# Optimization experiments

Hardware: AMD Instinct MI355X
Metric: run time of the kernel (lower is better)

Reference implementation:

```python
import jax, jax.numpy as jnp
from jax import lax
import numpy as np

B, P, M1, M2, M3 = 128, 168, 2, 2, 2
M = M1 * M2 * M3
HIDC, HIDR, HIDS, CK, SKIP, HW = 50, 50, 5, 6, 24, 24
PT = (P - CK) // SKIP  # int((P-Ck)/skip) = 6
L = P - CK + 1         # 163


def gru(xs, w_ih, w_hh, b_ih, b_hh, hid):
    # xs: [T, N, in]; torch nn.GRU cell semantics, h0 = 0. Returns final h: [N, hid].
    def step(h, x):
        gi = x @ w_ih.T + b_ih
        gh = h @ w_hh.T + b_hh
        ir, iz, inn = jnp.split(gi, 3, axis=-1)
        hr, hz, hn = jnp.split(gh, 3, axis=-1)
        r = jax.nn.sigmoid(ir + hr)
        z = jax.nn.sigmoid(iz + hz)
        n = jnp.tanh(inn + r * hn)
        return (1.0 - z) * n + z * h, None
    h0 = jnp.zeros((xs.shape[1], hid), xs.dtype)
    h, _ = lax.scan(step, h0, xs)
    return h


def setup_inputs() -> dict:
    key = jax.random.key(0)
    ks = jax.random.split(key, 16)
    O = P * HIDC * CK  # 50400 conv output channels
    d = {
        'x': jax.random.normal(ks[0], (B, P, M1, M2, M3), jnp.float32),
        'conv_w': jax.random.normal(ks[1], (O, P, M1, M2, M3), jnp.float32) * 0.02,
        'conv_b': jax.random.normal(ks[2], (O,), jnp.float32) * 0.02,
        'g1_wih': jax.random.normal(ks[3], (3 * HIDR, HIDC), jnp.float32) * 0.1,
        'g1_whh': jax.random.normal(ks[4], (3 * HIDR, HIDR), jnp.float32) * 0.1,
        'g1_bih': jax.random.normal(ks[5], (3 * HIDR,), jnp.float32) * 0.1,
        'g1_bhh': jax.random.normal(ks[6], (3 * HIDR,), jnp.float32) * 0.1,
        'gs_wih': jax.random.normal(ks[7], (3 * HIDS, HIDC), jnp.float32) * 0.1,
        'gs_whh': jax.random.normal(ks[8], (3 * HIDS, HIDS), jnp.float32) * 0.1,
        'gs_bih': jax.random.normal(ks[9], (3 * HIDS,), jnp.float32) * 0.1,
        'gs_bhh': jax.random.normal(ks[10], (3 * HIDS,), jnp.float32) * 0.1,
        'l1_w': jax.random.normal(ks[11], (M, HIDR + SKIP * HIDS), jnp.float32) * 0.1,
        'l1_b': jax.random.normal(ks[12], (M,), jnp.float32) * 0.1,
        'hw_w': jax.random.normal(ks[13], (1, HW), jnp.float32) * 0.1,
        'hw_b': jax.random.normal(ks[14], (1,), jnp.float32) * 0.1,
    }
    return d


def reference(x, conv_w, conv_b, g1_wih, g1_whh, g1_bih, g1_bhh,
              gs_wih, gs_whh, gs_bih, gs_bhh, l1_w, l1_b, hw_w, hw_b):
    # Conv3d with kernel == full spatial extent is a dense matmul over (P*m1*m2*m3).
    xf = x.reshape(B, -1)                       # [B, P*M]
    wf = conv_w.reshape(conv_w.shape[0], -1)    # [O, P*M]
    c = jax.nn.relu(xf @ wf.T + conv_b)         # [B, O]
    c = c.reshape(B, HIDC, CK, P)
    # Diagonal strided sum (the torch triple loop): res1[b,c,t] = sum_k c[b,c,k,k+t]
    res1 = sum(c[:, :, k, k:k + L] for k in range(CK))  # [B, HIDC, L]
    # dropout: eval mode (identity)
    r = gru(jnp.transpose(res1, (2, 0, 1)), g1_wih, g1_whh, g1_bih, g1_bhh, HIDR)  # [B, HIDR]
    # skip GRU
    s = res1[:, :, -PT * SKIP:]                          # [B, HIDC, PT*SKIP]
    s = s.reshape(B, HIDC, PT, SKIP)
    s = jnp.transpose(s, (2, 0, 3, 1)).reshape(PT, B * SKIP, HIDC)
    hs = gru(s, gs_wih, gs_whh, gs_bih, gs_bhh, HIDS)    # [B*SKIP, HIDS]
    hs = hs.reshape(B, SKIP * HIDS)
    r = jnp.concatenate([r, hs], axis=1)                 # [B, HIDR + SKIP*HIDS]
    res = r @ l1_w.T + l1_b                              # [B, M]
    # highway (AR) component over the last HW timesteps
    z = x[:, -HW:].reshape(B, HW, M)                     # [B, HW, M]
    z = jnp.transpose(z, (0, 2, 1)).reshape(-1, HW)      # [B*M, HW]
    z = z @ hw_w.T + hw_b                                # [B*M, 1]
    res = res + z.reshape(B, M)
    res = jax.nn.sigmoid(res)
    return res.reshape(B, M1, M2, M3)
```

## Files before the change

### kernel.cpp

```cpp
#include <hip/hip_runtime.h>
#include <hip/hip_bf16.h>
#include <cstdint>


typedef __attribute__((ext_vector_type(8))) short short8;
typedef __attribute__((ext_vector_type(4))) float f32x4;

__device__ __forceinline__ unsigned short bf16rn(float f) {
    unsigned u = __float_as_uint(f);
    return (unsigned short)((u + 0x7FFFu + ((u >> 16) & 1u)) >> 16);
}
__device__ __forceinline__ unsigned pk2(float a, float b) {
    return ((unsigned)bf16rn(b) << 16) | (unsigned)bf16rn(a);
}
__device__ __forceinline__ uint4 pack8(float4 f0, float4 f1) {
    uint4 u;
    u.x = pk2(f0.x, f0.y); u.y = pk2(f0.z, f0.w);
    u.z = pk2(f1.x, f1.y); u.w = pk2(f1.z, f1.w);
    return u;
}
__device__ __forceinline__ float bf2f(unsigned short u) {
    return __uint_as_float((unsigned)u << 16);
}
__device__ __forceinline__ float sigmf(float x) { return 1.f / (1.f + __expf(-x)); }
__device__ __forceinline__ float tanhf_(float x) { return 1.f - 2.f / (__expf(2.f * x) + 1.f); }

__global__ __launch_bounds__(256, 2)
void k1_conv_gemm(const float* __restrict__ x, const float* __restrict__ w,
                  const float* __restrict__ bias, unsigned short* __restrict__ c) {
    __shared__ uint4 a_lds[8 * 129];
    __shared__ uint4 b_lds[8 * 113];
    const int tid  = threadIdx.x;
    const int n0   = blockIdx.x * 112;
    const int wave = tid >> 6, lane = tid & 63;
    const int quad = lane >> 4, m16 = lane & 15;

    f32x4 acc[2][7];
#pragma unroll
    for (int i = 0; i < 2; ++i)
#pragma unroll
        for (int j = 0; j < 7; ++j) acc[i][j] = (f32x4){0.f, 0.f, 0.f, 0.f};

    for (int kb = 0; kb < 1344; kb += 64) {
#pragma unroll
        for (int i = 0; i < 4; ++i) {
            int idx = tid + i * 256;
            int row = idx >> 3, ks = idx & 7;
            const float* gp = x + row * 1344 + kb + ks * 8;
            float4 f0 = *reinterpret_cast<const float4*>(gp);
            float4 f1 = *reinterpret_cast<const float4*>(gp + 4);
            a_lds[ks * 129 + row] = pack8(f0, f1);
        }
#pragma unroll
        for (int i = 0; i < 4; ++i) {
            int idx = tid + i * 256;
            if (idx < 896) {
                int row = idx >> 3, ks = idx & 7;
                const float* gp = w + (size_t)(n0 + row) * 1344 + kb + ks * 8;
                float4 f0 = *reinterpret_cast<const float4*>(gp);
                float4 f1 = *reinterpret_cast<const float4*>(gp + 4);
                b_lds[ks * 113 + row] = pack8(f0, f1);
            }
        }
        __syncthreads();
#pragma unroll
        for (int half = 0; half < 2; ++half) {
            const int kp = half * 4 + quad;
            short8 af[2], bfr[7];
#pragma unroll
            for (int rt = 0; rt < 2; ++rt)
                af[rt] = ((const short8*)a_lds)[kp * 129 + wave * 32 + rt * 16 + m16];
#pragma unroll
            for (int ct = 0; ct < 7; ++ct)
                bfr[ct] = ((const short8*)b_lds)[kp * 113 + ct * 16 + m16];
#pragma unroll
            for (int rt = 0; rt < 2; ++rt)
#pragma unroll
                for (int ct = 0; ct < 7; ++ct)
                    acc[rt][ct] = __builtin_amdgcn_mfma_f32_16x16x32_bf16(
                        af[rt], bfr[ct], acc[rt][ct], 0, 0, 0);
        }
        __syncthreads();
    }
#pragma unroll
    for (int ct = 0; ct < 7; ++ct) {
        int col = n0 + ct * 16 + m16;
        float bv = bias[col];
#pragma unroll
        for (int rt = 0; rt < 2; ++rt) {
#pragma unroll
            for (int r = 0; r < 4; ++r) {
                int grow = wave * 32 + rt * 16 + quad * 4 + r;
                float v = acc[rt][ct][r] + bv;
                v = fmaxf(v, 0.f);
                c[(size_t)grow * 50400 + col] = bf16rn(v);
            }
        }
    }
}

__global__ __launch_bounds__(256)
void k2_diag(const unsigned short* __restrict__ c, float* __restrict__ res1) {
    __shared__ float rloc[50 * 164];
    const int b = blockIdx.x;
    const unsigned short* cb = c + (size_t)b * 50400;
    for (int idx = threadIdx.x; idx < 8150; idx += 256) {
        int hc = idx / 163, t = idx - hc * 163;
        int base = hc * 1008 + t;
        float s = 0.f;
#pragma unroll
        for (int k = 0; k < 6; ++k) s += bf2f(cb[base + 169 * k]);
        rloc[hc * 164 + t] = s;
    }
    __syncthreads();
    for (int idx = threadIdx.x; idx < 8150; idx += 256) {
        int t = idx / 50, hc = idx - t * 50;
        res1[(size_t)(t * 128 + b) * 50 + hc] = rloc[hc * 164 + t];
    }
}

__global__ __launch_bounds__(256)
void k3_gi1(const float* __restrict__ res1, const float* __restrict__ wih,
            const float* __restrict__ bih, float* __restrict__ gi1) {
    __shared__ float wl[150 * 51];
    __shared__ float xl[32 * 50];
    const int row0 = blockIdx.x * 32;
    for (int idx = threadIdx.x; idx < 7500; idx += 256) {
        int r = idx / 50, j = idx - r * 50;
        wl[r * 51 + j] = wih[idx];
    }
    for (int idx = threadIdx.x; idx < 1600; idx += 256)
        xl[idx] = res1[(size_t)row0 * 50 + idx];
    __syncthreads();
    for (int e = threadIdx.x; e < 4800; e += 256) {
        int rr = e / 150, cc = e - rr * 150;
        float acc = bih[cc];
        const float* xp = &xl[rr * 50];
        const float* wp = &wl[cc * 51];
#pragma unroll
        for (int j = 0; j < 50; ++j) acc += xp[j] * wp[j];
        gi1[(size_t)(row0 + rr) * 150 + cc] = acc;
    }
}

__global__ __launch_bounds__(256)
void k3_gi2(const float* __restrict__ res1, const float* __restrict__ wih,
            const float* __restrict__ bih, float* __restrict__ gi2) {
    __shared__ float wl[15 * 51];
    __shared__ float xl[32 * 50];
    const int row0 = blockIdx.x * 32;
    for (int idx = threadIdx.x; idx < 750; idx += 256) {
        int r = idx / 50, j = idx - r * 50;
        wl[r * 51 + j] = wih[idx];
    }
    for (int idx = threadIdx.x; idx < 1600; idx += 256) {
        int rr = idx / 50, j = idx - rr * 50;
        int r = row0 + rr;
        int pt = r / 3072, bsk = r - pt * 3072;
        int b = bsk / 24, sk = bsk - b * 24;
        int t = 19 + pt * 24 + sk;
        xl[idx] = res1[(size_t)(t * 128 + b) * 50 + j];
    }
    __syncthreads();
    for (int e = threadIdx.x; e < 480; e += 256) {
        int rr = e / 15, cc = e - rr * 15;
        float acc = bih[cc];
#pragma unroll
        for (int j = 0; j < 50; ++j) acc += xl[rr * 50 + j] * wl[cc * 51 + j];
        gi2[(size_t)(row0 + rr) * 15 + cc] = acc;
    }
}

__global__ __launch_bounds__(64)
void k4_gru1(const float* __restrict__ gi1, const float* __restrict__ whh,
             const float* __restrict__ bhh, float* __restrict__ r1) {
    __shared__ float wl[7500];
    __shared__ __align__(16) float hl[52];
    const int b = blockIdx.x;
    const int l = threadIdx.x;
    for (int idx = l; idx < 7500; idx += 64) wl[idx] = whh[idx];
    if (l < 52) hl[l] = 0.f;
    __syncthreads();
    const int lc = (l < 50) ? l : 49;
    float wr[50], wz[50], wn[50];
#pragma unroll
    for (int j = 0; j < 50; ++j) {
        wr[j] = wl[lc * 50 + j];
        wz[j] = wl[(50 + lc) * 50 + j];
        wn[j] = wl[(100 + lc) * 50 + j];
    }
    const float bhr = bhh[lc], bhz = bhh[50 + lc], bhn = bhh[100 + lc];
    float hcur = 0.f;
    for (int t = 0; t < 163; ++t) {
        const float* gp = gi1 + ((size_t)t * 128 + b) * 150;
        float gir = gp[lc], giz = gp[50 + lc], gin = gp[100 + lc];
        float ar = bhr, az = bhz, an = bhn;
#pragma unroll
        for (int j4 = 0; j4 < 12; ++j4) {
            float4 hv = *reinterpret_cast<const float4*>(&hl[4 * j4]);
            ar += wr[4 * j4 + 0] * hv.x + wr[4 * j4 + 1] * hv.y +
                  wr[4 * j4 + 2] * hv.z + wr[4 * j4 + 3] * hv.w;
            az += wz[4 * j4 + 0] * hv.x + wz[4 * j4 + 1] * hv.y +
                  wz[4 * j4 + 2] * hv.z + wz[4 * j4 + 3] * hv.w;
            an += wn[4 * j4 + 0] * hv.x + wn[4 * j4 + 1] * hv.y +
                  wn[4 * j4 + 2] * hv.z + wn[4 * j4 + 3] * hv.w;
        }
        {
            float h48 = hl[48], h49 = hl[49];
            ar += wr[48] * h48 + wr[49] * h49;
            az += wz[48] * h48 + wz[49] * h49;
            an += wn[48] * h48 + wn[49] * h49;
        }
        float rg = sigmf(gir + ar);
        float zg = sigmf(giz + az);
        float ng = tanhf_(gin + rg * an);
        float hn = (1.f - zg) * ng + zg * hcur;
        __syncthreads();
        if (l < 50) { hl[l] = hn; hcur = hn; }
        __syncthreads();
    }
    if (l < 50) r1[b * 50 + l] = hcur;
}

__global__ __launch_bounds__(256)
void k5_gru2(const float* __restrict__ gi2, const float* __restrict__ whh,
             const float* __restrict__ bhh, float* __restrict__ hs) {
    __shared__ float wl[75];
    __shared__ float bl[15];
    const int tid = threadIdx.x;
    if (tid < 75) wl[tid] = whh[tid];
    if (tid < 15) bl[tid] = bhh[tid];
    __syncthreads();
    const int bsk = blockIdx.x * 256 + tid;
    float h[5] = {0.f, 0.f, 0.f, 0.f, 0.f};
    for (int pt = 0; pt < 6; ++pt) {
        const float* gp = gi2 + (size_t)(pt * 3072 + bsk) * 15;
        float gi[15];
#pragma unroll
        for (int i = 0; i < 15; ++i) gi[i] = gp[i];
        float gh[15];
#pragma unroll
        for (int i = 0; i < 15; ++i) {
            float s = bl[i];
#pragma unroll
            for (int j = 0; j < 5; ++j) s += wl[i * 5 + j] * h[j];
            gh[i] = s;
        }
#pragma unroll
        for (int u = 0; u < 5; ++u) {
            float rg = sigmf(gi[u] + gh[u]);
            float zg = sigmf(gi[5 + u] + gh[5 + u]);
            float ng = tanhf_(gi[10 + u] + rg * gh[10 + u]);
            h[u] = (1.f - zg) * ng + zg * h[u];
        }
    }
#pragma unroll
    for (int u = 0; u < 5; ++u) hs[bsk * 5 + u] = h[u];
}

__global__ __launch_bounds__(256)
void k6_final(const float* __restrict__ r1, const float* __restrict__ hs,
              const float* __restrict__ l1w, const float* __restrict__ l1b,
              const float* __restrict__ x, const float* __restrict__ hww,
              const float* __restrict__ hwb, float* __restrict__ out) {
    const int tid = blockIdx.x * 256 + threadIdx.x;
    if (tid >= 1024) return;
    const int b = tid >> 3, m = tid & 7;
    float acc = l1b[m];
    const float* wrow = l1w + m * 170;
    const float* rb = r1 + b * 50;
#pragma unroll
    for (int j = 0; j < 50; ++j) acc += rb[j] * wrow[j];
    const float* hb = hs + b * 120;
#pragma unroll
    for (int j = 0; j < 120; ++j) acc += hb[j] * wrow[50 + j];
    float z = hwb[0];
    const float* xb = x + b * 1344 + 144 * 8 + m;
#pragma unroll
    for (int wi = 0; wi < 24; ++wi) z += xb[wi * 8] * hww[wi];
    out[tid] = 1.f / (1.f + __expf(-(acc + z)));
}

extern "C" void kernel_launch(void* const* d_in, const int* in_sizes, int n_in,
                              void* d_out, int out_size, void* d_ws, size_t ws_size,
                              hipStream_t stream) {
    const float* x      = (const float*)d_in[0];
    const float* conv_w = (const float*)d_in[1];
    const float* conv_b = (const float*)d_in[2];
    const float* g1_wih = (const float*)d_in[3];
    const float* g1_whh = (const float*)d_in[4];
    const float* g1_bih = (const float*)d_in[5];
    const float* g1_bhh = (const float*)d_in[6];
    const float* gs_wih = (const float*)d_in[7];
    const float* gs_whh = (const float*)d_in[8];
    const float* gs_bih = (const float*)d_in[9];
    const float* gs_bhh = (const float*)d_in[10];
    const float* l1_w   = (const float*)d_in[11];
    const float* l1_b   = (const float*)d_in[12];
    const float* hw_w   = (const float*)d_in[13];
    const float* hw_b   = (const float*)d_in[14];
    float* out = (float*)d_out;

    char* ws = (char*)d_ws;
    unsigned short* c   = (unsigned short*)(ws);
    float* res1         = (float*)(ws + 12902400);
    float* gi1          = (float*)(ws + 17075200);
    float* gi2          = (float*)(ws + 29593600);
    float* r1           = (float*)(ws + 30699520);
    float* hs           = (float*)(ws + 30725120);

    hipLaunchKernelGGL(k1_conv_gemm, dim3(450), dim3(256), 0, stream, x, conv_w, conv_b, c);
    hipLaunchKernelGGL(k2_diag,      dim3(128), dim3(256), 0, stream, c, res1);
    hipLaunchKernelGGL(k3_gi1,       dim3(652), dim3(256), 0, stream, res1, g1_wih, g1_bih, gi1);
    hipLaunchKernelGGL(k3_gi2,       dim3(576), dim3(256), 0, stream, res1, gs_wih, gs_bih, gi2);
    hipLaunchKernelGGL(k4_gru1,      dim3(128), dim3(64),  0, stream, gi1, g1_whh, g1_bhh, r1);
    hipLaunchKernelGGL(k5_gru2,      dim3(12),  dim3(256), 0, stream, gi2, gs_whh, gs_bhh, hs);
    hipLaunchKernelGGL(k6_final,     dim3(4),   dim3(256), 0, stream, r1, hs, l1_w, l1_b, x, hw_w, hw_b, out);
}
```

Before: 618.0 us.

## Prefetch GEMM tiles into registers, vectorize input projections, double-buffer GRU hidden state

The conv GEMM now loads the next K-tile from global memory into registers while MFMAs run on the current tile, hiding load latency behind compute at the cost of more registers. The input-projection kernels process 64 rows per block with float4-vectorized dot products over padded LDS rows. The GRU1 recurrence double-buffers the hidden state to drop one barrier per step and prefetches the next step's gate inputs. Register pressure in the GEMM could reduce occupancy, and the changed summation order slightly alters floating-point results.

After: 588.1 us. 4.8% less time.

```diff
diff --git a/kernel.cpp b/kernel.cpp
--- a/kernel.cpp
+++ b/kernel.cpp
@@ -41,28 +41,47 @@
 #pragma unroll
         for (int j = 0; j < 7; ++j) acc[i][j] = (f32x4){0.f, 0.f, 0.f, 0.f};
 
+    float4 pa[4][2];
+    float4 pb[4][2];
+
+    auto issue = [&](int kb) {
+#pragma unroll
+        for (int i = 0; i < 4; ++i) {
+            int row = (tid >> 3) + 32 * i;
+            const float* gp = x + row * 1344 + kb + (tid & 7) * 8;
+            pa[i][0] = *reinterpret_cast<const float4*>(gp);
+            pa[i][1] = *reinterpret_cast<const float4*>(gp + 4);
+        }
+#pragma unroll
+        for (int i = 0; i < 4; ++i) {
+            int idx = tid + 256 * i;
+            if (idx < 896) {
+                int row = idx >> 3;
+                const float* gp = w + (size_t)(n0 + row) * 1344 + kb + (idx & 7) * 8;
+                pb[i][0] = *reinterpret_cast<const float4*>(gp);
+                pb[i][1] = *reinterpret_cast<const float4*>(gp + 4);
+            }
+        }
+    };
+
+    issue(0);
     for (int kb = 0; kb < 1344; kb += 64) {
 #pragma unroll
         for (int i = 0; i < 4; ++i) {
-            int idx = tid + i * 256;
+            int idx = tid + 256 * i;
             int row = idx >> 3, ks = idx & 7;
-            const float* gp = x + row * 1344 + kb + ks * 8;
-            float4 f0 = *reinterpret_cast<const float4*>(gp);
-            float4 f1 = *reinterpret_cast<const float4*>(gp + 4);
-            a_lds[ks * 129 + row] = pack8(f0, f1);
+            a_lds[ks * 129 + row] = pack8(pa[i][0], pa[i][1]);
         }
 #pragma unroll
         for (int i = 0; i < 4; ++i) {
-            int idx = tid + i * 256;
+            int idx = tid + 256 * i;
             if (idx < 896) {
                 int row = idx >> 3, ks = idx & 7;
-                const float* gp = w + (size_t)(n0 + row) * 1344 + kb + ks * 8;
-                float4 f0 = *reinterpret_cast<const float4*>(gp);
-                float4 f1 = *reinterpret_cast<const float4*>(gp + 4);
-                b_lds[ks * 113 + row] = pack8(f0, f1);
+                b_lds[ks * 113 + row] = pack8(pb[i][0], pb[i][1]);
             }
         }
         __syncthreads();
+        if (kb + 64 < 1344) issue(kb + 64);
 #pragma unroll
         for (int half = 0; half < 2; ++half) {
             const int kp = half * 4 + quad;
@@ -122,23 +141,32 @@
 __global__ __launch_bounds__(256)
 void k3_gi1(const float* __restrict__ res1, const float* __restrict__ wih,
             const float* __restrict__ bih, float* __restrict__ gi1) {
-    __shared__ float wl[150 * 51];
-    __shared__ float xl[32 * 50];
-    const int row0 = blockIdx.x * 32;
+    __shared__ float wl[150 * 52];
+    __shared__ float xl[64 * 52];
+    const int row0 = blockIdx.x * 64;
     for (int idx = threadIdx.x; idx < 7500; idx += 256) {
         int r = idx / 50, j = idx - r * 50;
-        wl[r * 51 + j] = wih[idx];
-    }
-    for (int idx = threadIdx.x; idx < 1600; idx += 256)
-        xl[idx] = res1[(size_t)row0 * 50 + idx];
-    __syncthreads();
-    for (int e = threadIdx.x; e < 4800; e += 256) {
+        wl[r * 52 + j] = wih[idx];
+    }
+    for (int idx = threadIdx.x; idx < 3200; idx += 256) {
+        int r = idx / 50, j = idx - r * 50;
+        xl[r * 52 + j] = res1[(size_t)row0 * 50 + idx];
+    }
+    __syncthreads();
+    for (int e = threadIdx.x; e < 9600; e += 256) {
         int rr = e / 150, cc = e - rr * 150;
-        float acc = bih[cc];
-        const float* xp = &xl[rr * 50];
-        const float* wp = &wl[cc * 51];
-#pragma unroll
-        for (int j = 0; j < 50; ++j) acc += xp[j] * wp[j];
+        float4 a0 = {0.f, 0.f, 0.f, 0.f};
+        const float* xp = &xl[rr * 52];
+        const float* wp = &wl[cc * 52];
+#pragma unroll
+        for (int j = 0; j < 48; j += 4) {
+            float4 xv = *reinterpret_cast<const float4*>(xp + j);
+            float4 wv = *reinterpret_cast<const float4*>(wp + j);
+            a0.x += xv.x * wv.x; a0.y += xv.y * wv.y;
+            a0.z += xv.z * wv.z; a0.w += xv.w * wv.w;
+        }
+        float acc = bih[cc] + xp[48] * wp[48] + xp[49] * wp[49]
+                  + (a0.x + a0.y) + (a0.z + a0.w);
         gi1[(size_t)(row0 + rr) * 150 + cc] = acc;
     }
 }
@@ -146,27 +174,36 @@
 __global__ __launch_bounds__(256)
 void k3_gi2(const float* __restrict__ res1, const float* __restrict__ wih,
             const float* __restrict__ bih, float* __restrict__ gi2) {
-    __shared__ float wl[15 * 51];
-    __shared__ float xl[32 * 50];
-    const int row0 = blockIdx.x * 32;
+    __shared__ float wl[15 * 52];
+    __shared__ float xl[64 * 52];
+    const int row0 = blockIdx.x * 64;
     for (int idx = threadIdx.x; idx < 750; idx += 256) {
         int r = idx / 50, j = idx - r * 50;
-        wl[r * 51 + j] = wih[idx];
-    }
-    for (int idx = threadIdx.x; idx < 1600; idx += 256) {
+        wl[r * 52 + j] = wih[idx];
+    }
+    for (int idx = threadIdx.x; idx < 3200; idx += 256) {
         int rr = idx / 50, j = idx - rr * 50;
         int r = row0 + rr;
         int pt = r / 3072, bsk = r - pt * 3072;
         int b = bsk / 24, sk = bsk - b * 24;
         int t = 19 + pt * 24 + sk;
-        xl[idx] = res1[(size_t)(t * 128 + b) * 50 + j];
-    }
-    __syncthreads();
-    for (int e = threadIdx.x; e < 480; e += 256) {
+        xl[rr * 52 + j] = res1[(size_t)(t * 128 + b) * 50 + j];
+    }
+    __syncthreads();
+    for (int e = threadIdx.x; e < 960; e += 256) {
         int rr = e / 15, cc = e - rr * 15;
-        float acc = bih[cc];
-#pragma unroll
-        for (int j = 0; j < 50; ++j) acc += xl[rr * 50 + j] * wl[cc * 51 + j];
+        float4 a0 = {0.f, 0.f, 0.f, 0.f};
+        const float* xp = &xl[rr * 52];
+        const float* wp = &wl[cc * 52];
+#pragma unroll
+        for (int j = 0; j < 48; j += 4) {
+            float4 xv = *reinterpret_cast<const float4*>(xp + j);
+            float4 wv = *reinterpret_cast<const float4*>(wp + j);
+            a0.x += xv.x * wv.x; a0.y += xv.y * wv.y;
+            a0.z += xv.z * wv.z; a0.w += xv.w * wv.w;
+        }
+        float acc = bih[cc] + xp[48] * wp[48] + xp[49] * wp[49]
+                  + (a0.x + a0.y) + (a0.z + a0.w);
         gi2[(size_t)(row0 + rr) * 15 + cc] = acc;
     }
 }
@@ -175,11 +212,12 @@
 void k4_gru1(const float* __restrict__ gi1, const float* __restrict__ whh,
              const float* __restrict__ bhh, float* __restrict__ r1) {
     __shared__ float wl[7500];
-    __shared__ __align__(16) float hl[52];
+    __shared__ __align__(16) float hl[2][64];
     const int b = blockIdx.x;
     const int l = threadIdx.x;
     for (int idx = l; idx < 7500; idx += 64) wl[idx] = whh[idx];
-    if (l < 52) hl[l] = 0.f;
+    hl[0][l] = 0.f;
+    hl[1][l] = 0.f;
     __syncthreads();
     const int lc = (l < 50) ? l : 49;
     float wr[50], wz[50], wn[50];
@@ -191,13 +229,20 @@
     }
     const float bhr = bhh[lc], bhz = bhh[50 + lc], bhn = bhh[100 + lc];
     float hcur = 0.f;
+    const float* gp = gi1 + (size_t)b * 150;
+    float gir = gp[lc], giz = gp[50 + lc], gin = gp[100 + lc];
+    int p = 0;
     for (int t = 0; t < 163; ++t) {
-        const float* gp = gi1 + ((size_t)t * 128 + b) * 150;
-        float gir = gp[lc], giz = gp[50 + lc], gin = gp[100 + lc];
+        float ngir = 0.f, ngiz = 0.f, ngin = 0.f;
+        if (t < 162) {
+            const float* gq = gp + 150 * 128;
+            ngir = gq[lc]; ngiz = gq[50 + lc]; ngin = gq[100 + lc];
+        }
+        const float* hp = hl[p];
         float ar = bhr, az = bhz, an = bhn;
 #pragma unroll
         for (int j4 = 0; j4 < 12; ++j4) {
-            float4 hv = *reinterpret_cast<const float4*>(&hl[4 * j4]);
+            float4 hv = *reinterpret_cast<const float4*>(hp + 4 * j4);
             ar += wr[4 * j4 + 0] * hv.x + wr[4 * j4 + 1] * hv.y +
                   wr[4 * j4 + 2] * hv.z + wr[4 * j4 + 3] * hv.w;
             az += wz[4 * j4 + 0] * hv.x + wz[4 * j4 + 1] * hv.y +
@@ -206,7 +251,7 @@
                   wn[4 * j4 + 2] * hv.z + wn[4 * j4 + 3] * hv.w;
         }
         {
-            float h48 = hl[48], h49 = hl[49];
+            float h48 = hp[48], h49 = hp[49];
             ar += wr[48] * h48 + wr[49] * h49;
             az += wz[48] * h48 + wz[49] * h49;
             an += wn[48] * h48 + wn[49] * h49;
@@ -215,9 +260,12 @@
         float zg = sigmf(giz + az);
         float ng = tanhf_(gin + rg * an);
         float hn = (1.f - zg) * ng + zg * hcur;
+        hl[1 - p][l] = hn;
         __syncthreads();
-        if (l < 50) { hl[l] = hn; hcur = hn; }
-        __syncthreads();
+        p ^= 1;
+        hcur = hn;
+        gir = ngir; giz = ngiz; gin = ngin;
+        gp += 150 * 128;
     }
     if (l < 50) r1[b * 50 + l] = hcur;
 }
@@ -311,8 +359,8 @@
 
     hipLaunchKernelGGL(k1_conv_gemm, dim3(450), dim3(256), 0, stream, x, conv_w, conv_b, c);
     hipLaunchKernelGGL(k2_diag,      dim3(128), dim3(256), 0, stream, c, res1);
-    hipLaunchKernelGGL(k3_gi1,       dim3(652), dim3(256), 0, stream, res1, g1_wih, g1_bih, gi1);
-    hipLaunchKernelGGL(k3_gi2,       dim3(576), dim3(256), 0, stream, res1, gs_wih, gs_bih, gi2);
+    hipLaunchKernelGGL(k3_gi1,       dim3(326), dim3(256), 0, stream, res1, g1_wih, g1_bih, gi1);
+    hipLaunchKernelGGL(k3_gi2,       dim3(288), dim3(256), 0, stream, res1, gs_wih, gs_bih, gi2);
     hipLaunchKernelGGL(k4_gru1,      dim3(128), dim3(64),  0, stream, gi1, g1_whh, g1_bhh, r1);
     hipLaunchKernelGGL(k5_gru2,      dim3(12),  dim3(256), 0, stream, gi2, gs_whh, gs_bhh, hs);
     hipLaunchKernelGGL(k6_final,     dim3(4),   dim3(256), 0, stream, r1, hs, l1_w, l1_b, x, hw_w, hw_b, out);
```
